# Optimization experiments

Measured on AMD Instinct MI355X. Metric: run time of the kernel, lower is better.

## Reference

```python
import jax, jax.numpy as jnp
import numpy as np

E, N, D, OUT = 1_600_000, 50_000, 128, 128
EPS_STD = 1e-5
EPS_BN = 1e-5


def setup_inputs() -> dict:
    key = jax.random.key(0)
    k0, k1, k2, k3 = jax.random.split(key, 4)
    inputs = jax.random.normal(k0, (E, D), dtype=jnp.float32)
    index = jax.random.randint(k1, (E,), 0, N, dtype=jnp.int32)
    # learned params
    deg_emb = jax.random.normal(k2, (100, D), dtype=jnp.float32) * 0.02  # nn.Embedding(100, nin)
    W = jax.random.normal(k3, (5 * D, OUT), dtype=jnp.float32) / np.sqrt(5 * D)  # bias-free Linear
    gamma = jnp.ones((OUT,), jnp.float32)   # BatchNorm1d weight
    beta = jnp.zeros((OUT,), jnp.float32)   # BatchNorm1d bias
    return {"inputs": inputs, "index": index, "deg_emb": deg_emb,
            "W": W, "gamma": gamma, "beta": beta, "dim_size": N}


def _aggregate(inputs, index, deg_emb, dim_size):
    ones = jnp.ones((inputs.shape[0],), inputs.dtype)
    cnt = jax.ops.segment_sum(ones, index, num_segments=dim_size)          # [N]
    safe = jnp.maximum(cnt, 1.0)[:, None]                                   # torch_scatter mean clamps count>=1
    s = jax.ops.segment_sum(inputs, index, num_segments=dim_size)          # [N, D]
    sq = jax.ops.segment_sum(inputs * inputs, index, num_segments=dim_size)
    mean = s / safe
    mean_sq = sq / safe
    mn = jax.ops.segment_min(inputs, index, num_segments=dim_size)
    mx = jax.ops.segment_max(inputs, index, num_segments=dim_size)
    has = (cnt > 0)[:, None]
    mn = jnp.where(has, mn, 0.0)  # empty segments -> 0 like torch_scatter
    mx = jnp.where(has, mx, 0.0)
    std = jnp.sqrt(jax.nn.relu(mean_sq - mean * mean) + EPS_STD)
    deg = jnp.minimum(cnt.astype(jnp.int32), 99)  # degree embedding lookup (table size 100)
    return jnp.concatenate([mean, mn, mx, std, deg_emb[deg]], axis=-1)     # [N, 5D]


def reference(inputs, index, deg_emb, W, gamma, beta, dim_size):
    x = _aggregate(inputs, index, deg_emb, dim_size)
    h = x @ W                                      # Linear, no bias
    mu = h.mean(axis=0)
    var = h.var(axis=0)                            # biased, as BatchNorm training mode
    h = (h - mu) / jnp.sqrt(var + EPS_BN) * gamma + beta
    return jax.nn.relu(h)
```

## Files before the change

### kernel.cpp

```cpp
#include <hip/hip_runtime.h>
#include <cstdint>
#include <cstddef>

#define NNODES 50000
#define DIM 128
#define K5 640
#define OUTD 128
#define MPAD 50048
#define EPS_STD 1e-5f
#define EPS_BN 1e-5f
#define LDA 40
#define LDB 40

typedef __attribute__((ext_vector_type(8))) __bf16 bf16x8;
typedef __attribute__((ext_vector_type(4))) float f32x4;

__device__ __forceinline__ unsigned short f2bf(float f) {
  unsigned int u = __float_as_uint(f);
  u = u + 0x7fffu + ((u >> 16) & 1u);
  return (unsigned short)(u >> 16);
}

__global__ void hist_k(const int* __restrict__ idx, int* __restrict__ counts, int E) {
  int e = blockIdx.x * 256 + threadIdx.x;
  if (e < E) atomicAdd(&counts[idx[e]], 1);
}

__global__ void scan1_k(const int* __restrict__ counts, int* __restrict__ offsets,
                        int* __restrict__ blocksums, int n) {
  __shared__ int sh[256];
  int t = threadIdx.x;
  int i = blockIdx.x * 256 + t;
  int v = (i < n) ? counts[i] : 0;
  sh[t] = v; __syncthreads();
  for (int off = 1; off < 256; off <<= 1) {
    int add = (t >= off) ? sh[t - off] : 0;
    __syncthreads();
    sh[t] += add;
    __syncthreads();
  }
  if (i < n) offsets[i] = sh[t] - v;
  if (t == 255) blocksums[blockIdx.x] = sh[t];
}

__global__ void scan2_k(int* __restrict__ blocksums, int nb) {
  __shared__ int sh[256];
  int t = threadIdx.x;
  int v = (t < nb) ? blocksums[t] : 0;
  sh[t] = v; __syncthreads();
  for (int off = 1; off < 256; off <<= 1) {
    int add = (t >= off) ? sh[t - off] : 0;
    __syncthreads();
    sh[t] += add;
    __syncthreads();
  }
  if (t < nb) blocksums[t] = sh[t] - v;
}

__global__ void scan3_k(int* __restrict__ offsets, const int* __restrict__ blocksums,
                        int* __restrict__ cursor, int n) {
  int i = blockIdx.x * 256 + threadIdx.x;
  if (i < n) {
    int o = offsets[i] + blocksums[blockIdx.x];
    offsets[i] = o;
    cursor[i] = o;
  }
}

__global__ void scatter_k(const int* __restrict__ idx, int* __restrict__ cursor,
                          int* __restrict__ sorted, int E) {
  int e = blockIdx.x * 256 + threadIdx.x;
  if (e < E) {
    int p = atomicAdd(&cursor[idx[e]], 1);
    sorted[p] = e;
  }
}

__global__ void convW_k(const float* __restrict__ W, unsigned short* __restrict__ Wt) {
  int t = blockIdx.x * 256 + threadIdx.x;
  if (t >= OUTD * K5) return;
  int c = t / K5, k = t % K5;
  Wt[t] = f2bf(W[(size_t)k * OUTD + c]);
}

__global__ __launch_bounds__(256) void agg_k(
    const float* __restrict__ inp, const int* __restrict__ sorted,
    const int* __restrict__ offsets, const int* __restrict__ counts,
    const float* __restrict__ deg_emb, unsigned short* __restrict__ x) {
  const int wid  = threadIdx.x >> 6;
  const int node = blockIdx.x * 4 + wid;
  const int lane = threadIdx.x & 63;
  const int half = lane >> 5;
  const int sl   = lane & 31;
  const int c0   = sl * 4;
  unsigned short* xrow = x + (size_t)node * K5;

  if (node >= NNODES) {
    if (half == 0) {
      ushort4 z = {0, 0, 0, 0};
      #pragma unroll
      for (int sgm = 0; sgm < 5; sgm++) *(ushort4*)(xrow + sgm * DIM + c0) = z;
    }
    return;
  }

  const int start = offsets[node];
  const int cnt   = counts[node];
  float s[4] = {0.f, 0.f, 0.f, 0.f}, q[4] = {0.f, 0.f, 0.f, 0.f};
  float mn[4], mx[4];
  #pragma unroll
  for (int i = 0; i < 4; i++) { mn[i] = INFINITY; mx[i] = -INFINITY; }

  for (int j0 = 0; j0 < cnt; j0 += 64) {
    const int lim = min(64, cnt - j0);
    int myid = 0;
    if (j0 + lane < cnt) myid = sorted[start + j0 + lane];
    int j = 0;
    for (; j + 8 <= lim; j += 8) {
      const int e0 = __shfl(myid, j + 0 + half);
      const int e1 = __shfl(myid, j + 2 + half);
      const int e2 = __shfl(myid, j + 4 + half);
      const int e3 = __shfl(myid, j + 6 + half);
      const float4 a0 = *(const float4*)(inp + (size_t)e0 * DIM + c0);
      const float4 a1 = *(const float4*)(inp + (size_t)e1 * DIM + c0);
      const float4 a2 = *(const float4*)(inp + (size_t)e2 * DIM + c0);
      const float4 a3 = *(const float4*)(inp + (size_t)e3 * DIM + c0);
      const float v0[4] = {a0.x, a0.y, a0.z, a0.w};
      const float v1[4] = {a1.x, a1.y, a1.z, a1.w};
      const float v2[4] = {a2.x, a2.y, a2.z, a2.w};
      const float v3[4] = {a3.x, a3.y, a3.z, a3.w};
      #pragma unroll
      for (int i = 0; i < 4; i++) {
        s[i] += v0[i] + v1[i] + v2[i] + v3[i];
        q[i] += v0[i] * v0[i] + v1[i] * v1[i] + v2[i] * v2[i] + v3[i] * v3[i];
        mn[i] = fminf(fminf(fminf(mn[i], v0[i]), fminf(v1[i], v2[i])), v3[i]);
        mx[i] = fmaxf(fmaxf(fmaxf(mx[i], v0[i]), fmaxf(v1[i], v2[i])), v3[i]);
      }
    }
    for (; j < lim; j += 2) {
      const int r = j + half;
      const int e = __shfl(myid, r < lim ? r : (lim - 1));
      if (r < lim) {
        const float4 a = *(const float4*)(inp + (size_t)e * DIM + c0);
        const float v[4] = {a.x, a.y, a.z, a.w};
        #pragma unroll
        for (int i = 0; i < 4; i++) {
          s[i] += v[i];
          q[i] += v[i] * v[i];
          mn[i] = fminf(mn[i], v[i]);
          mx[i] = fmaxf(mx[i], v[i]);
        }
      }
    }
  }
  #pragma unroll
  for (int i = 0; i < 4; i++) {
    s[i] += __shfl_xor(s[i], 32);
    q[i] += __shfl_xor(q[i], 32);
    mn[i] = fminf(mn[i], __shfl_xor(mn[i], 32));
    mx[i] = fmaxf(mx[i], __shfl_xor(mx[i], 32));
  }
  if (half) return;

  const float inv = 1.0f / (float)max(cnt, 1);
  const int deg = min(cnt, 99);
  const float4 e4 = *(const float4*)(deg_emb + (size_t)deg * DIM + c0);
  const float emb[4] = {e4.x, e4.y, e4.z, e4.w};
  float mean[4], sd[4];
  #pragma unroll
  for (int i = 0; i < 4; i++) {
    mean[i] = s[i] * inv;
    float var = q[i] * inv - mean[i] * mean[i];
    sd[i] = sqrtf(fmaxf(var, 0.f) + EPS_STD);
    if (cnt == 0) { mn[i] = 0.f; mx[i] = 0.f; }
  }
  { ushort4 u = {f2bf(mean[0]), f2bf(mean[1]), f2bf(mean[2]), f2bf(mean[3])};
    *(ushort4*)(xrow + 0 * DIM + c0) = u; }
  { ushort4 u = {f2bf(mn[0]), f2bf(mn[1]), f2bf(mn[2]), f2bf(mn[3])};
    *(ushort4*)(xrow + 1 * DIM + c0) = u; }
  { ushort4 u = {f2bf(mx[0]), f2bf(mx[1]), f2bf(mx[2]), f2bf(mx[3])};
    *(ushort4*)(xrow + 2 * DIM + c0) = u; }
  { ushort4 u = {f2bf(sd[0]), f2bf(sd[1]), f2bf(sd[2]), f2bf(sd[3])};
    *(ushort4*)(xrow + 3 * DIM + c0) = u; }
  { ushort4 u = {f2bf(emb[0]), f2bf(emb[1]), f2bf(emb[2]), f2bf(emb[3])};
    *(ushort4*)(xrow + 4 * DIM + c0) = u; }
}

__global__ __launch_bounds__(256) void gemm_k(const unsigned short* __restrict__ x,
                                              const unsigned short* __restrict__ Wt,
                                              float* __restrict__ h,
                                              float* __restrict__ colsum,
                                              float* __restrict__ colsumsq) {
  __shared__ unsigned short As[64 * LDA];
  __shared__ unsigned short Bs[128 * LDB];
  __shared__ float sh_s[4 * 128];
  __shared__ float sh_q[4 * 128];
  const int t = threadIdx.x;
  const int m0 = blockIdx.x * 64;
  const int w = t >> 6, lane = t & 63;
  const int lm = lane & 15, lq = lane >> 4;

  f32x4 acc[8];
  #pragma unroll
  for (int i = 0; i < 8; i++) acc[i] = (f32x4){0.f, 0.f, 0.f, 0.f};

  const int arow = t >> 2, akoff = (t & 3) * 8;
  const int bt0 = t * 8, bt1 = 2048 + t * 8;
  const int bc0 = bt0 >> 5, bk0 = bt0 & 31;
  const int bc1 = bt1 >> 5, bk1 = bt1 & 31;

  for (int k0 = 0; k0 < K5; k0 += 32) {
    *(uint4*)&As[arow * LDA + akoff] = *(const uint4*)&x[(size_t)(m0 + arow) * K5 + k0 + akoff];
    *(uint4*)&Bs[bc0 * LDB + bk0]    = *(const uint4*)&Wt[(size_t)bc0 * K5 + k0 + bk0];
    *(uint4*)&Bs[bc1 * LDB + bk1]    = *(const uint4*)&Wt[(size_t)bc1 * K5 + k0 + bk1];
    __syncthreads();
    const bf16x8 a = *(const bf16x8*)&As[(w * 16 + lm) * LDA + lq * 8];
    #pragma unroll
    for (int tt = 0; tt < 8; tt++) {
      const bf16x8 b = *(const bf16x8*)&Bs[(tt * 16 + lm) * LDB + lq * 8];
      acc[tt] = __builtin_amdgcn_mfma_f32_16x16x32_bf16(a, b, acc[tt], 0, 0, 0);
    }
    __syncthreads();
  }
  float psum[8], psq[8];
  #pragma unroll
  for (int tt = 0; tt < 8; tt++) {
    psum[tt] = 0.f; psq[tt] = 0.f;
    #pragma unroll
    for (int r = 0; r < 4; r++) {
      const int row = m0 + w * 16 + lq * 4 + r;
      if (row < NNODES) {
        const float v = acc[tt][r];
        h[(size_t)row * OUTD + tt * 16 + lm] = v;
        psum[tt] += v;
        psq[tt]  += v * v;
      }
    }
  }
  #pragma unroll
  for (int tt = 0; tt < 8; tt++) {
    psum[tt] += __shfl_xor(psum[tt], 16);
    psum[tt] += __shfl_xor(psum[tt], 32);
    psq[tt]  += __shfl_xor(psq[tt], 16);
    psq[tt]  += __shfl_xor(psq[tt], 32);
  }
  if (lq == 0) {
    #pragma unroll
    for (int tt = 0; tt < 8; tt++) {
      sh_s[w * 128 + tt * 16 + lm] = psum[tt];
      sh_q[w * 128 + tt * 16 + lm] = psq[tt];
    }
  }
  __syncthreads();
  if (t < 128) {
    float s = sh_s[t] + sh_s[128 + t] + sh_s[256 + t] + sh_s[384 + t];
    float qv = sh_q[t] + sh_q[128 + t] + sh_q[256 + t] + sh_q[384 + t];
    atomicAdd(&colsum[t], s);
    atomicAdd(&colsumsq[t], qv);
  }
}

__global__ void norm_k(float* __restrict__ h, const float* __restrict__ colsum,
                       const float* __restrict__ colsumsq, const float* __restrict__ gamma,
                       const float* __restrict__ beta) {
  const int i = blockIdx.x * 256 + threadIdx.x;
  const int total = NNODES * OUTD / 4;
  if (i >= total) return;
  const int c0 = (i * 4) & (OUTD - 1);
  const float invN = 1.0f / (float)NNODES;
  float4 v = *(const float4*)(h + (size_t)i * 4);
  float out[4] = {v.x, v.y, v.z, v.w};
  #pragma unroll
  for (int j = 0; j < 4; j++) {
    const int c = c0 + j;
    const float mu = colsum[c] * invN;
    const float var = colsumsq[c] * invN - mu * mu;
    const float rs = rsqrtf(var + EPS_BN);
    const float tv = (out[j] - mu) * rs * gamma[c] + beta[c];
    out[j] = fmaxf(tv, 0.f);
  }
  float4 o4 = {out[0], out[1], out[2], out[3]};
  *(float4*)(h + (size_t)i * 4) = o4;
}

extern "C" void kernel_launch(void* const* d_in, const int* in_sizes, int n_in,
                              void* d_out, int out_size, void* d_ws, size_t ws_size,
                              hipStream_t stream) {
  const float* inputs  = (const float*)d_in[0];
  const int*   index   = (const int*)d_in[1];
  const float* deg_emb = (const float*)d_in[2];
  const float* W       = (const float*)d_in[3];
  const float* gamma   = (const float*)d_in[4];
  const float* beta    = (const float*)d_in[5];
  const int E = in_sizes[1];

  char* ws = (char*)d_ws;
  size_t o = 0;
  int* counts = (int*)(ws + o);       o += (size_t)NNODES * 4;
  float* colsum = (float*)(ws + o);   o += 128 * 4;
  float* colsumsq = (float*)(ws + o); o += 128 * 4;
  const size_t zero_bytes = o;
  o = (o + 255) & ~(size_t)255;
  int* offsets = (int*)(ws + o);      o += (size_t)NNODES * 4;
  o = (o + 255) & ~(size_t)255;
  int* cursor = (int*)(ws + o);       o += (size_t)NNODES * 4;
  o = (o + 255) & ~(size_t)255;
  int* blocksums = (int*)(ws + o);    o += 256 * 4;
  o = (o + 255) & ~(size_t)255;
  int* sorted = (int*)(ws + o);       o += (size_t)E * 4;
  o = (o + 255) & ~(size_t)255;
  unsigned short* Wt = (unsigned short*)(ws + o); o += (size_t)OUTD * K5 * 2;
  o = (o + 255) & ~(size_t)255;
  unsigned short* x = (unsigned short*)(ws + o);  o += (size_t)MPAD * K5 * 2;

  float* h = (float*)d_out;

  hipMemsetAsync(counts, 0, zero_bytes, stream);
  hist_k<<<(E + 255) / 256, 256, 0, stream>>>(index, counts, E);
  const int NB = (NNODES + 255) / 256;
  scan1_k<<<NB, 256, 0, stream>>>(counts, offsets, blocksums, NNODES);
  scan2_k<<<1, 256, 0, stream>>>(blocksums, NB);
  scan3_k<<<NB, 256, 0, stream>>>(offsets, blocksums, cursor, NNODES);
  scatter_k<<<(E + 255) / 256, 256, 0, stream>>>(index, cursor, sorted, E);
  convW_k<<<(OUTD * K5 + 255) / 256, 256, 0, stream>>>(W, Wt);
  agg_k<<<MPAD / 4, 256, 0, stream>>>(inputs, sorted, offsets, counts, deg_emb, x);
  gemm_k<<<MPAD / 64, 256, 0, stream>>>(x, Wt, h, colsum, colsumsq);
  norm_k<<<(NNODES * OUTD / 4 + 255) / 256, 256, 0, stream>>>(h, colsum, colsumsq, gamma, beta);
}
```

Measured before the change: 1.319 ms.

## Fuse segment aggregation and GEMM into one kernel via LDS-resident feature tile

Merges the aggregation kernel and the bf16 MFMA GEMM into a single 512-thread kernel. Each block aggregates 64 nodes into a full 64x640 bf16 tile in shared memory, then multiplies it with Wt read directly from global/L2. This removes the round trip of the 64MB intermediate x through HBM and one kernel launch. In exchange, launch bounds (512,1) and roughly 100KB of LDS limit occupancy, so fewer waves are available to hide the gather latency of the aggregation phase. Only 782 blocks run, which may balance poorly across CUs.

```diff
diff --git a/kernel.cpp b/kernel.cpp
--- a/kernel.cpp
+++ b/kernel.cpp
@@ -7,10 +7,10 @@
 #define K5 640
 #define OUTD 128
 #define MPAD 50048
+#define NBLK 782
 #define EPS_STD 1e-5f
 #define EPS_BN 1e-5f
 #define LDA 40
-#define LDB 40
 
 typedef __attribute__((ext_vector_type(8))) __bf16 bf16x8;
 typedef __attribute__((ext_vector_type(4))) float f32x4;
@@ -83,180 +83,187 @@
   Wt[t] = f2bf(W[(size_t)k * OUTD + c]);
 }
 
-__global__ __launch_bounds__(256) void agg_k(
+__global__ __launch_bounds__(512, 1) void fused_k(
     const float* __restrict__ inp, const int* __restrict__ sorted,
     const int* __restrict__ offsets, const int* __restrict__ counts,
-    const float* __restrict__ deg_emb, unsigned short* __restrict__ x) {
-  const int wid  = threadIdx.x >> 6;
-  const int node = blockIdx.x * 4 + wid;
-  const int lane = threadIdx.x & 63;
-  const int half = lane >> 5;
-  const int sl   = lane & 31;
-  const int c0   = sl * 4;
-  unsigned short* xrow = x + (size_t)node * K5;
-
-  if (node >= NNODES) {
-    if (half == 0) {
-      ushort4 z = {0, 0, 0, 0};
+    const float* __restrict__ deg_emb, const unsigned short* __restrict__ Wt,
+    float* __restrict__ h, float* __restrict__ colsum, float* __restrict__ colsumsq) {
+  __shared__ unsigned short As[20 * 64 * LDA];
+  __shared__ float sh_s[8 * 64];
+  __shared__ float sh_q[8 * 64];
+
+  const int t    = threadIdx.x;
+  const int wv   = t >> 6;
+  const int lane = t & 63;
+  const int m0   = blockIdx.x * 64;
+
+  {
+    const int half = lane >> 5;
+    const int sl   = lane & 31;
+    const int c0   = sl * 4;
+    const int wc   = sl >> 3;
+    const int wkk  = (sl & 7) * 4;
+
+    for (int i = 0; i < 8; i++) {
+      const int r    = wv * 8 + i;
+      const int node = m0 + r;
+
+      if (node >= NNODES) {
+        if (half == 0) {
+          ushort4 z = {0, 0, 0, 0};
+          #pragma unroll
+          for (int sgm = 0; sgm < 5; sgm++) {
+            const int c = sgm * 4 + wc;
+            *(ushort4*)&As[(c * 64 + r) * LDA + wkk] = z;
+          }
+        }
+        continue;
+      }
+
+      const int start = offsets[node];
+      const int cnt   = counts[node];
+      float s[4] = {0.f, 0.f, 0.f, 0.f}, q[4] = {0.f, 0.f, 0.f, 0.f};
+      float mn[4], mx[4];
       #pragma unroll
-      for (int sgm = 0; sgm < 5; sgm++) *(ushort4*)(xrow + sgm * DIM + c0) = z;
-    }
-    return;
-  }
-
-  const int start = offsets[node];
-  const int cnt   = counts[node];
-  float s[4] = {0.f, 0.f, 0.f, 0.f}, q[4] = {0.f, 0.f, 0.f, 0.f};
-  float mn[4], mx[4];
+      for (int k = 0; k < 4; k++) { mn[k] = INFINITY; mx[k] = -INFINITY; }
+
+      for (int j0 = 0; j0 < cnt; j0 += 64) {
+        const int lim = min(64, cnt - j0);
+        int myid = 0;
+        if (j0 + lane < cnt) myid = sorted[start + j0 + lane];
+        int j = 0;
+        for (; j + 8 <= lim; j += 8) {
+          const int e0 = __shfl(myid, j + 0 + half);
+          const int e1 = __shfl(myid, j + 2 + half);
+          const int e2 = __shfl(myid, j + 4 + half);
+          const int e3 = __shfl(myid, j + 6 + half);
+          const float4 a0 = *(const float4*)(inp + (size_t)e0 * DIM + c0);
+          const float4 a1 = *(const float4*)(inp + (size_t)e1 * DIM + c0);
+          const float4 a2 = *(const float4*)(inp + (size_t)e2 * DIM + c0);
+          const float4 a3 = *(const float4*)(inp + (size_t)e3 * DIM + c0);
+          const float v0[4] = {a0.x, a0.y, a0.z, a0.w};
+          const float v1[4] = {a1.x, a1.y, a1.z, a1.w};
+          const float v2[4] = {a2.x, a2.y, a2.z, a2.w};
+          const float v3[4] = {a3.x, a3.y, a3.z, a3.w};
+          #pragma unroll
+          for (int k = 0; k < 4; k++) {
+            s[k] += v0[k] + v1[k] + v2[k] + v3[k];
+            q[k] += v0[k] * v0[k] + v1[k] * v1[k] + v2[k] * v2[k] + v3[k] * v3[k];
+            mn[k] = fminf(fminf(fminf(mn[k], v0[k]), fminf(v1[k], v2[k])), v3[k]);
+            mx[k] = fmaxf(fmaxf(fmaxf(mx[k], v0[k]), fmaxf(v1[k], v2[k])), v3[k]);
+          }
+        }
+        for (; j < lim; j += 2) {
+          const int rr = j + half;
+          const int e = __shfl(myid, rr < lim ? rr : (lim - 1));
+          if (rr < lim) {
+            const float4 a = *(const float4*)(inp + (size_t)e * DIM + c0);
+            const float v[4] = {a.x, a.y, a.z, a.w};
+            #pragma unroll
+            for (int k = 0; k < 4; k++) {
+              s[k] += v[k];
+              q[k] += v[k] * v[k];
+              mn[k] = fminf(mn[k], v[k]);
+              mx[k] = fmaxf(mx[k], v[k]);
+            }
+          }
+        }
+      }
+      #pragma unroll
+      for (int k = 0; k < 4; k++) {
+        s[k] += __shfl_xor(s[k], 32);
+        q[k] += __shfl_xor(q[k], 32);
+        mn[k] = fminf(mn[k], __shfl_xor(mn[k], 32));
+        mx[k] = fmaxf(mx[k], __shfl_xor(mx[k], 32));
+      }
+
+      if (half == 0) {
+        const float inv = 1.0f / (float)max(cnt, 1);
+        const int deg = min(cnt, 99);
+        const float4 e4 = *(const float4*)(deg_emb + (size_t)deg * DIM + c0);
+        const float emb[4] = {e4.x, e4.y, e4.z, e4.w};
+        float mean[4], sd[4];
+        #pragma unroll
+        for (int k = 0; k < 4; k++) {
+          mean[k] = s[k] * inv;
+          float var = q[k] * inv - mean[k] * mean[k];
+          sd[k] = sqrtf(fmaxf(var, 0.f) + EPS_STD);
+          if (cnt == 0) { mn[k] = 0.f; mx[k] = 0.f; }
+        }
+        const ushort4 seg[5] = {
+          {f2bf(mean[0]), f2bf(mean[1]), f2bf(mean[2]), f2bf(mean[3])},
+          {f2bf(mn[0]),   f2bf(mn[1]),   f2bf(mn[2]),   f2bf(mn[3])},
+          {f2bf(mx[0]),   f2bf(mx[1]),   f2bf(mx[2]),   f2bf(mx[3])},
+          {f2bf(sd[0]),   f2bf(sd[1]),   f2bf(sd[2]),   f2bf(sd[3])},
+          {f2bf(emb[0]),  f2bf(emb[1]),  f2bf(emb[2]),  f2bf(emb[3])}};
+        #pragma unroll
+        for (int sgm = 0; sgm < 5; sgm++) {
+          const int c = sgm * 4 + wc;
+          *(ushort4*)&As[(c * 64 + r) * LDA + wkk] = seg[sgm];
+        }
+      }
+    }
+  }
+  __syncthreads();
+
+  const int lm = lane & 15, lq = lane >> 4;
+  const int rs = wv & 3;
+  const int ch = wv >> 2;
+
+  f32x4 acc[4];
   #pragma unroll
-  for (int i = 0; i < 4; i++) { mn[i] = INFINITY; mx[i] = -INFINITY; }
-
-  for (int j0 = 0; j0 < cnt; j0 += 64) {
-    const int lim = min(64, cnt - j0);
-    int myid = 0;
-    if (j0 + lane < cnt) myid = sorted[start + j0 + lane];
-    int j = 0;
-    for (; j + 8 <= lim; j += 8) {
-      const int e0 = __shfl(myid, j + 0 + half);
-      const int e1 = __shfl(myid, j + 2 + half);
-      const int e2 = __shfl(myid, j + 4 + half);
-      const int e3 = __shfl(myid, j + 6 + half);
-      const float4 a0 = *(const float4*)(inp + (size_t)e0 * DIM + c0);
-      const float4 a1 = *(const float4*)(inp + (size_t)e1 * DIM + c0);
-      const float4 a2 = *(const float4*)(inp + (size_t)e2 * DIM + c0);
-      const float4 a3 = *(const float4*)(inp + (size_t)e3 * DIM + c0);
-      const float v0[4] = {a0.x, a0.y, a0.z, a0.w};
-      const float v1[4] = {a1.x, a1.y, a1.z, a1.w};
-      const float v2[4] = {a2.x, a2.y, a2.z, a2.w};
-      const float v3[4] = {a3.x, a3.y, a3.z, a3.w};
-      #pragma unroll
-      for (int i = 0; i < 4; i++) {
-        s[i] += v0[i] + v1[i] + v2[i] + v3[i];
-        q[i] += v0[i] * v0[i] + v1[i] * v1[i] + v2[i] * v2[i] + v3[i] * v3[i];
-        mn[i] = fminf(fminf(fminf(mn[i], v0[i]), fminf(v1[i], v2[i])), v3[i]);
-        mx[i] = fmaxf(fmaxf(fmaxf(mx[i], v0[i]), fmaxf(v1[i], v2[i])), v3[i]);
-      }
-    }
-    for (; j < lim; j += 2) {
-      const int r = j + half;
-      const int e = __shfl(myid, r < lim ? r : (lim - 1));
-      if (r < lim) {
-        const float4 a = *(const float4*)(inp + (size_t)e * DIM + c0);
-        const float v[4] = {a.x, a.y, a.z, a.w};
-        #pragma unroll
-        for (int i = 0; i < 4; i++) {
-          s[i] += v[i];
-          q[i] += v[i] * v[i];
-          mn[i] = fminf(mn[i], v[i]);
-          mx[i] = fmaxf(mx[i], v[i]);
-        }
-      }
-    }
-  }
+  for (int i = 0; i < 4; i++) acc[i] = (f32x4){0.f, 0.f, 0.f, 0.f};
+
+  #pragma unroll 4
+  for (int c = 0; c < 20; c++) {
+    const bf16x8 a = *(const bf16x8*)&As[(c * 64 + rs * 16 + lm) * LDA + lq * 8];
+    #pragma unroll
+    for (int tt = 0; tt < 4; tt++) {
+      const bf16x8 b = *(const bf16x8*)&Wt[(size_t)(ch * 64 + tt * 16 + lm) * K5 + c * 32 + lq * 8];
+      acc[tt] = __builtin_amdgcn_mfma_f32_16x16x32_bf16(a, b, acc[tt], 0, 0, 0);
+    }
+  }
+
+  float psum[4], psq[4];
   #pragma unroll
-  for (int i = 0; i < 4; i++) {
-    s[i] += __shfl_xor(s[i], 32);
-    q[i] += __shfl_xor(q[i], 32);
-    mn[i] = fminf(mn[i], __shfl_xor(mn[i], 32));
-    mx[i] = fmaxf(mx[i], __shfl_xor(mx[i], 32));
-  }
-  if (half) return;
-
-  const float inv = 1.0f / (float)max(cnt, 1);
-  const int deg = min(cnt, 99);
-  const float4 e4 = *(const float4*)(deg_emb + (size_t)deg * DIM + c0);
-  const float emb[4] = {e4.x, e4.y, e4.z, e4.w};
-  float mean[4], sd[4];
-  #pragma unroll
-  for (int i = 0; i < 4; i++) {
-    mean[i] = s[i] * inv;
-    float var = q[i] * inv - mean[i] * mean[i];
-    sd[i] = sqrtf(fmaxf(var, 0.f) + EPS_STD);
-    if (cnt == 0) { mn[i] = 0.f; mx[i] = 0.f; }
-  }
-  { ushort4 u = {f2bf(mean[0]), f2bf(mean[1]), f2bf(mean[2]), f2bf(mean[3])};
-    *(ushort4*)(xrow + 0 * DIM + c0) = u; }
-  { ushort4 u = {f2bf(mn[0]), f2bf(mn[1]), f2bf(mn[2]), f2bf(mn[3])};
-    *(ushort4*)(xrow + 1 * DIM + c0) = u; }
-  { ushort4 u = {f2bf(mx[0]), f2bf(mx[1]), f2bf(mx[2]), f2bf(mx[3])};
-    *(ushort4*)(xrow + 2 * DIM + c0) = u; }
-  { ushort4 u = {f2bf(sd[0]), f2bf(sd[1]), f2bf(sd[2]), f2bf(sd[3])};
-    *(ushort4*)(xrow + 3 * DIM + c0) = u; }
-  { ushort4 u = {f2bf(emb[0]), f2bf(emb[1]), f2bf(emb[2]), f2bf(emb[3])};
-    *(ushort4*)(xrow + 4 * DIM + c0) = u; }
-}
-
-__global__ __launch_bounds__(256) void gemm_k(const unsigned short* __restrict__ x,
-                                              const unsigned short* __restrict__ Wt,
-                                              float* __restrict__ h,
-                                              float* __restrict__ colsum,
-                                              float* __restrict__ colsumsq) {
-  __shared__ unsigned short As[64 * LDA];
-  __shared__ unsigned short Bs[128 * LDB];
-  __shared__ float sh_s[4 * 128];
-  __shared__ float sh_q[4 * 128];
-  const int t = threadIdx.x;
-  const int m0 = blockIdx.x * 64;
-  const int w = t >> 6, lane = t & 63;
-  const int lm = lane & 15, lq = lane >> 4;
-
-  f32x4 acc[8];
-  #pragma unroll
-  for (int i = 0; i < 8; i++) acc[i] = (f32x4){0.f, 0.f, 0.f, 0.f};
-
-  const int arow = t >> 2, akoff = (t & 3) * 8;
-  const int bt0 = t * 8, bt1 = 2048 + t * 8;
-  const int bc0 = bt0 >> 5, bk0 = bt0 & 31;
-  const int bc1 = bt1 >> 5, bk1 = bt1 & 31;
-
-  for (int k0 = 0; k0 < K5; k0 += 32) {
-    *(uint4*)&As[arow * LDA + akoff] = *(const uint4*)&x[(size_t)(m0 + arow) * K5 + k0 + akoff];
-    *(uint4*)&Bs[bc0 * LDB + bk0]    = *(const uint4*)&Wt[(size_t)bc0 * K5 + k0 + bk0];
-    *(uint4*)&Bs[bc1 * LDB + bk1]    = *(const uint4*)&Wt[(size_t)bc1 * K5 + k0 + bk1];
-    __syncthreads();
-    const bf16x8 a = *(const bf16x8*)&As[(w * 16 + lm) * LDA + lq * 8];
-    #pragma unroll
-    for (int tt = 0; tt < 8; tt++) {
-      const bf16x8 b = *(const bf16x8*)&Bs[(tt * 16 + lm) * LDB + lq * 8];
-      acc[tt] = __builtin_amdgcn_mfma_f32_16x16x32_bf16(a, b, acc[tt], 0, 0, 0);
-    }
-    __syncthreads();
-  }
-  float psum[8], psq[8];
-  #pragma unroll
-  for (int tt = 0; tt < 8; tt++) {
+  for (int tt = 0; tt < 4; tt++) {
     psum[tt] = 0.f; psq[tt] = 0.f;
     #pragma unroll
-    for (int r = 0; r < 4; r++) {
-      const int row = m0 + w * 16 + lq * 4 + r;
+    for (int rr = 0; rr < 4; rr++) {
+      const int row = m0 + rs * 16 + lq * 4 + rr;
       if (row < NNODES) {
-        const float v = acc[tt][r];
-        h[(size_t)row * OUTD + tt * 16 + lm] = v;
+        const float v = acc[tt][rr];
+        h[(size_t)row * OUTD + ch * 64 + tt * 16 + lm] = v;
         psum[tt] += v;
         psq[tt]  += v * v;
       }
     }
   }
   #pragma unroll
-  for (int tt = 0; tt < 8; tt++) {
+  for (int tt = 0; tt < 4; tt++) {
     psum[tt] += __shfl_xor(psum[tt], 16);
     psum[tt] += __shfl_xor(psum[tt], 32);
     psq[tt]  += __shfl_xor(psq[tt], 16);
     psq[tt]  += __shfl_xor(psq[tt], 32);
   }
-  if (lq == 0) {
+  if (lane < 16) {
     #pragma unroll
-    for (int tt = 0; tt < 8; tt++) {
-      sh_s[w * 128 + tt * 16 + lm] = psum[tt];
-      sh_q[w * 128 + tt * 16 + lm] = psq[tt];
+    for (int tt = 0; tt < 4; tt++) {
+      sh_s[wv * 64 + tt * 16 + lane] = psum[tt];
+      sh_q[wv * 64 + tt * 16 + lane] = psq[tt];
     }
   }
   __syncthreads();
   if (t < 128) {
-    float s = sh_s[t] + sh_s[128 + t] + sh_s[256 + t] + sh_s[384 + t];
-    float qv = sh_q[t] + sh_q[128 + t] + sh_q[256 + t] + sh_q[384 + t];
-    atomicAdd(&colsum[t], s);
-    atomicAdd(&colsumsq[t], qv);
+    const int ch2 = t >> 6, local = t & 63;
+    float ss = 0.f, qq = 0.f;
+    #pragma unroll
+    for (int j = 0; j < 4; j++) {
+      ss += sh_s[(ch2 * 4 + j) * 64 + local];
+      qq += sh_q[(ch2 * 4 + j) * 64 + local];
+    }
+    atomicAdd(&colsum[t], ss);
+    atomicAdd(&colsumsq[t], qq);
   }
 }
 
@@ -310,8 +317,6 @@
   int* sorted = (int*)(ws + o);       o += (size_t)E * 4;
   o = (o + 255) & ~(size_t)255;
   unsigned short* Wt = (unsigned short*)(ws + o); o += (size_t)OUTD * K5 * 2;
-  o = (o + 255) & ~(size_t)255;
-  unsigned short* x = (unsigned short*)(ws + o);  o += (size_t)MPAD * K5 * 2;
 
   float* h = (float*)d_out;
 
@@ -323,7 +328,7 @@
   scan3_k<<<NB, 256, 0, stream>>>(offsets, blocksums, cursor, NNODES);
   scatter_k<<<(E + 255) / 256, 256, 0, stream>>>(index, cursor, sorted, E);
   convW_k<<<(OUTD * K5 + 255) / 256, 256, 0, stream>>>(W, Wt);
-  agg_k<<<MPAD / 4, 256, 0, stream>>>(inputs, sorted, offsets, counts, deg_emb, x);
-  gemm_k<<<MPAD / 64, 256, 0, stream>>>(x, Wt, h, colsum, colsumsq);
+  fused_k<<<NBLK, 512, 0, stream>>>(inputs, sorted, offsets, counts, deg_emb, Wt,
+                                    h, colsum, colsumsq);
   norm_k<<<(NNODES * OUTD / 4 + 255) / 256, 256, 0, stream>>>(h, colsum, colsumsq, gamma, beta);
 }
```

After: 1.403 ms. 1.06x slower.
